# Kernel optimization log

Measured on AMD Instinct MI355X. Metric: run time of the kernel, lower is better.

The kernel has to match this reference:

```python
import jax, jax.numpy as jnp
import numpy as np

E = 1_000_000      # number of edges
T = 2_000_000      # number of angle triplets
EDGE_DIM = 64
HIDDEN = 128
LN_EPS = 1e-5


def _layer_norm(x, gamma, beta):
    mu = jnp.mean(x, axis=-1, keepdims=True)
    var = jnp.mean(jnp.square(x - mu), axis=-1, keepdims=True)
    return (x - mu) * jax.lax.rsqrt(var + LN_EPS) * gamma + beta


def setup_inputs() -> dict:
    key = jax.random.key(0)
    ks = jax.random.split(key, 8)
    in_dim = 2 * EDGE_DIM + 4  # 132

    def lin(k, fan_in, fan_out):
        bound = 1.0 / np.sqrt(fan_in)
        kw, kb = jax.random.split(k)
        W = jax.random.uniform(kw, (fan_in, fan_out), jnp.float32, -bound, bound)
        b = jax.random.uniform(kb, (fan_out,), jnp.float32, -bound, bound)
        return W, b

    W1, b1 = lin(ks[0], in_dim, HIDDEN)
    W2, b2 = lin(ks[1], HIDDEN, HIDDEN)
    W3, b3 = lin(ks[2], HIDDEN, EDGE_DIM)

    return {
        "edge_feat": jax.random.normal(ks[3], (E, EDGE_DIM), jnp.float32),
        "triplet_idx": jax.random.randint(ks[4], (T, 2), 0, E, jnp.int64) if jax.config.jax_enable_x64 else jax.random.randint(ks[4], (T, 2), 0, E, jnp.int32),
        "triplet_geo": jax.random.uniform(ks[5], (T, 4), jnp.float32),
        "W1": W1, "b1": b1,
        "g1": jnp.ones((HIDDEN,), jnp.float32), "be1": jnp.zeros((HIDDEN,), jnp.float32),
        "W2": W2, "b2": b2,
        "g2": jnp.ones((HIDDEN,), jnp.float32), "be2": jnp.zeros((HIDDEN,), jnp.float32),
        "W3": W3, "b3": b3,
        "gn": jnp.ones((EDGE_DIM,), jnp.float32), "bn": jnp.zeros((EDGE_DIM,), jnp.float32),
    }


def reference(edge_feat, triplet_idx, triplet_geo,
              W1, b1, g1, be1, W2, b2, g2, be2, W3, b3, gn, bn):
    num_edges = edge_feat.shape[0]
    e_ij = triplet_idx[:, 0]
    e_kj = triplet_idx[:, 1]

    f_ij = edge_feat[e_ij]                      # [T, edge_dim] gather
    f_kj = edge_feat[e_kj]                      # [T, edge_dim] gather
    x = jnp.concatenate([f_ij, f_kj, triplet_geo], axis=1)  # [T, 2*edge_dim+4]

    # mlp_phi: Linear -> SiLU -> LayerNorm -> Linear -> SiLU -> LayerNorm
    h = _layer_norm(jax.nn.silu(x @ W1 + b1), g1, be1)
    m = _layer_norm(jax.nn.silu(h @ W2 + b2), g2, be2)  # [T, hidden]

    # scatter-mean over e_ij with dim_size = num_edges
    sums = jax.ops.segment_sum(m, e_ij, num_segments=num_edges)
    cnts = jax.ops.segment_sum(jnp.ones((m.shape[0],), m.dtype), e_ij, num_segments=num_edges)
    agg = sums / jnp.maximum(cnts, 1.0)[:, None]         # [E, hidden]

    out = edge_feat + (agg @ W3 + b3)
    return _layer_norm(out, gn, bn)
```

## Files before the change

### kernel.cpp

```cpp
#include <hip/hip_runtime.h>
#include <hip/hip_bf16.h>
#include <stdint.h>

typedef __attribute__((ext_vector_type(8))) short short8;
typedef __attribute__((ext_vector_type(4))) float f32x4;
typedef unsigned short u16;

#define OFF_PSUM 0ULL
#define OFF_CNT  256000000ULL
#define OFF_EBF  260000000ULL
#define OFF_WT1  388000000ULL
#define OFF_WT2  (OFF_WT1 + 40960ULL)
#define OFF_WP3  (OFF_WT2 + 32768ULL)
#define OFF_S2   (OFF_WP3 + 16384ULL)
#define OFF_C2   (OFF_S2 + 512ULL)
#define OFF_S3   (OFF_C2 + 512ULL)
#define OFF_T3   (OFF_S3 + 256ULL)

#define LDS_HM   0
#define LDS_TAIL 16384
#define LDS_P1S  20480
#define LDS_P1Q  20992
#define LDS_P2S  21504
#define LDS_P2Q  22016
#define LDS_EIJ  22528
#define LDS_TOTAL 22784

__device__ __forceinline__ u16 f2bf(float f) {
  union { float f; uint32_t u; } c; c.f = f;
  uint32_t u = c.u;
  return (u16)((u + 0x7FFFu + ((u >> 16) & 1u)) >> 16);
}
__device__ __forceinline__ uint32_t pkbf(float lo, float hi) {
  float2 t; t.x = lo; t.y = hi;
  __hip_bfloat162 h = __float22bfloat162_rn(t);
  uint32_t u; __builtin_memcpy(&u, &h, 4);
  return u;
}
__device__ __forceinline__ float silu(float y) {
  return y * __builtin_amdgcn_rcpf(1.0f + __expf(-y));
}

#define MFMA16(a, b, c) __builtin_amdgcn_mfma_f32_16x16x32_bf16((a), (b), (c), 0, 0, 0)


__global__ __launch_bounds__(256) void k_conv_edge(const float* __restrict__ ef,
                                                   u16* __restrict__ ebf) {
  int i = blockIdx.x * 256 + threadIdx.x;
  float4 v = ((const float4*)ef)[i];
  ushort4 o;
  o.x = f2bf(v.x); o.y = f2bf(v.y); o.z = f2bf(v.z); o.w = f2bf(v.w);
  ((ushort4*)ebf)[i] = o;
}

__global__ __launch_bounds__(256) void k_pack_w(const float* __restrict__ W1,
                                                const float* __restrict__ W2,
                                                const float* __restrict__ W3,
                                                const float* __restrict__ g1,
                                                const float* __restrict__ g2,
                                                u16* __restrict__ wt1,
                                                u16* __restrict__ wt2,
                                                u16* __restrict__ wp3) {
  int i = blockIdx.x * 256 + threadIdx.x;
  if (i < 20480) {
    int n = i / 160, k = i - n * 160;
    wt1[i] = (k < 132) ? f2bf(W1[k * 128 + n]) : (u16)0;
  } else if (i < 36864) {
    int i2 = i - 20480;
    int n = i2 >> 7, k = i2 & 127;
    wt2[i2] = f2bf(g1[k] * W2[k * 128 + n]);
  } else if (i < 45056) {
    int i3 = i - 36864;
    int j = i3 & 7, n = (i3 >> 3) & 63, kb = i3 >> 9;
    int k = kb * 8 + j;
    wp3[i3] = f2bf(g2[k] * W3[k * 64 + n]);
  }
}

__global__ __launch_bounds__(256) void k_pack_vec(
    const float* __restrict__ W2, const float* __restrict__ W3,
    const float* __restrict__ g1, const float* __restrict__ be1, const float* __restrict__ b2,
    const float* __restrict__ g2, const float* __restrict__ be2,
    float* __restrict__ s2, float* __restrict__ c2,
    float* __restrict__ s3, float* __restrict__ t3) {
  int t = threadIdx.x;
  if (t < 128) {
    float a = 0.f, b = 0.f;
    for (int k = 0; k < 128; ++k) {
      float w = W2[k * 128 + t];
      a += g1[k] * w; b += be1[k] * w;
    }
    s2[t] = a; c2[t] = b + b2[t];
  } else if (t < 192) {
    int n = t - 128;
    float a = 0.f, b = 0.f;
    for (int k = 0; k < 128; ++k) {
      float w = W3[k * 64 + n];
      a += g2[k] * w; b += be2[k] * w;
    }
    s3[n] = a; t3[n] = b;
  }
}


__global__ __launch_bounds__(256, 5) void k_triplet(
    const u16* __restrict__ ebf, const int* __restrict__ tidx,
    const float* __restrict__ geo,
    const u16* __restrict__ wt1, const u16* __restrict__ wt2, const u16* __restrict__ wp3,
    const float* __restrict__ b1,
    const float* __restrict__ s2v, const float* __restrict__ c2v,
    const float* __restrict__ s3v,
    float* __restrict__ psum, float* __restrict__ cnt) {
  __shared__ __align__(16) char smem[LDS_TOTAL];
  float* P1S = (float*)(smem + LDS_P1S);
  float* P1Q = (float*)(smem + LDS_P1Q);
  float* P2S = (float*)(smem + LDS_P2S);
  float* P2Q = (float*)(smem + LDS_P2Q);
  int* EIJ = (int*)(smem + LDS_EIJ);

  const int tid = threadIdx.x;
  const int wave = tid >> 6, lane = tid & 63;
  const int wm = wave >> 1, wn = wave & 1;
  const int l15 = lane & 15, lg = lane >> 4;
  const int t0 = blockIdx.x * 64;

  const int tA = wn * 32 + l15;
  const int tB = tA + 16;
  int2 pA = ((const int2*)tidx)[t0 + tA];
  int2 pB = ((const int2*)tidx)[t0 + tB];

  const short8* eb = (const short8*)ebf;
  short8 bxA0 = eb[(size_t)pA.x * 8 + lg];
  short8 bxA1 = eb[(size_t)pA.x * 8 + 4 + lg];
  short8 bxA2 = eb[(size_t)pA.y * 8 + lg];
  short8 bxA3 = eb[(size_t)pA.y * 8 + 4 + lg];
  short8 bxB0 = eb[(size_t)pB.x * 8 + lg];
  short8 bxB1 = eb[(size_t)pB.x * 8 + 4 + lg];
  short8 bxB2 = eb[(size_t)pB.y * 8 + lg];
  short8 bxB3 = eb[(size_t)pB.y * 8 + 4 + lg];

  if (tid < 64) {
    int2 p = ((const int2*)tidx)[t0 + tid];
    EIJ[tid] = p.x;
    atomicAdd(&cnt[p.x], 1.0f);
    float4 gq = ((const float4*)geo)[t0 + tid];
    uint2 gw; gw.x = pkbf(gq.x, gq.y); gw.y = pkbf(gq.z, gq.w);
    char* tp = smem + LDS_TAIL + tid * 64;
    const int ts = (tid & 3) << 4;
    *(uint2*)(tp + (0 ^ ts)) = gw;
    *(uint2*)(tp + (0 ^ ts) + 8) = (uint2){0, 0};
    *(uint4*)(tp + (16 ^ ts)) = (uint4){0, 0, 0, 0};
    *(uint4*)(tp + (32 ^ ts)) = (uint4){0, 0, 0, 0};
    *(uint4*)(tp + (48 ^ ts)) = (uint4){0, 0, 0, 0};
  }
  __syncthreads();

  short8 btA = *(const short8*)(smem + LDS_TAIL + tA * 64 + ((lg * 16) ^ ((tA & 3) << 4)));
  short8 btB = *(const short8*)(smem + LDS_TAIL + tB * 64 + ((lg * 16) ^ ((tB & 3) << 4)));

  f32x4 acc[4][2];
#pragma unroll
  for (int mf = 0; mf < 4; ++mf) { acc[mf][0] = (f32x4)0.f; acc[mf][1] = (f32x4)0.f; }
  const short8* w1p = (const short8*)wt1;
#pragma unroll
  for (int s5 = 0; s5 < 5; ++s5) {
    short8 b0, b1x;
    if (s5 == 0) { b0 = bxA0; b1x = bxB0; }
    else if (s5 == 1) { b0 = bxA1; b1x = bxB1; }
    else if (s5 == 2) { b0 = bxA2; b1x = bxB2; }
    else if (s5 == 3) { b0 = bxA3; b1x = bxB3; }
    else { b0 = btA; b1x = btB; }
#pragma unroll
    for (int mf = 0; mf < 4; ++mf) {
      short8 aw = w1p[(wm * 64 + mf * 16 + l15) * 20 + s5 * 4 + lg];
      acc[mf][0] = MFMA16(aw, b0, acc[mf][0]);
      acc[mf][1] = MFMA16(aw, b1x, acc[mf][1]);
    }
  }

  {
    float4 b1f[4];
#pragma unroll
    for (int mf = 0; mf < 4; ++mf)
      b1f[mf] = *(const float4*)(b1 + wm * 64 + mf * 16 + lg * 4);
    float st[2] = {0.f, 0.f}, sq[2] = {0.f, 0.f};
#pragma unroll
    for (int mf = 0; mf < 4; ++mf)
#pragma unroll
      for (int f = 0; f < 2; ++f)
#pragma unroll
        for (int q = 0; q < 4; ++q) {
          float v = silu(acc[mf][f][q] + b1f[mf][q]);
          acc[mf][f][q] = v;
          st[f] += v; sq[f] += v * v;
        }
#pragma unroll
    for (int f = 0; f < 2; ++f) {
      st[f] += __shfl_xor(st[f], 16); sq[f] += __shfl_xor(sq[f], 16);
      st[f] += __shfl_xor(st[f], 32); sq[f] += __shfl_xor(sq[f], 32);
    }
    if (lg == 0) {
#pragma unroll
      for (int f = 0; f < 2; ++f) {
        int trip = wn * 32 + f * 16 + l15;
        P1S[trip * 2 + wm] = st[f];
        P1Q[trip * 2 + wm] = sq[f];
      }
    }
#pragma unroll
    for (int mf = 0; mf < 4; ++mf)
#pragma unroll
      for (int f = 0; f < 2; ++f) {
        int trip = wn * 32 + f * 16 + l15;
        uint2 w;
        w.x = pkbf(acc[mf][f][0], acc[mf][f][1]);
        w.y = pkbf(acc[mf][f][2], acc[mf][f][3]);
        *(uint2*)(smem + LDS_HM + trip * 256 +
                  ((wm * 128 + mf * 32 + lg * 8) ^ ((trip & 7) << 4))) = w;
      }
  }
  __syncthreads();

#pragma unroll
  for (int mf = 0; mf < 4; ++mf) { acc[mf][0] = (f32x4)0.f; acc[mf][1] = (f32x4)0.f; }
  const short8* w2p = (const short8*)wt2;
#pragma unroll
  for (int s4 = 0; s4 < 4; ++s4) {
    short8 bx0, bx1;
    {
      int trip = wn * 32 + l15;
      bx0 = *(const short8*)(smem + LDS_HM + trip * 256 +
                             ((s4 * 64 + lg * 16) ^ ((trip & 7) << 4)));
      int trip2 = trip + 16;
      bx1 = *(const short8*)(smem + LDS_HM + trip2 * 256 +
                             ((s4 * 64 + lg * 16) ^ ((trip2 & 7) << 4)));
    }
#pragma unroll
    for (int mf = 0; mf < 4; ++mf) {
      short8 aw = w2p[(wm * 64 + mf * 16 + l15) * 16 + s4 * 4 + lg];
      acc[mf][0] = MFMA16(aw, bx0, acc[mf][0]);
      acc[mf][1] = MFMA16(aw, bx1, acc[mf][1]);
    }
  }

  {
    float4 s2f[4], c2f[4];
#pragma unroll
    for (int mf = 0; mf < 4; ++mf) {
      s2f[mf] = *(const float4*)(s2v + wm * 64 + mf * 16 + lg * 4);
      c2f[mf] = *(const float4*)(c2v + wm * 64 + mf * 16 + lg * 4);
    }
    float mu[2], inv[2];
#pragma unroll
    for (int f = 0; f < 2; ++f) {
      int trip = wn * 32 + f * 16 + l15;
      float sm = P1S[trip * 2] + P1S[trip * 2 + 1];
      float qq = P1Q[trip * 2] + P1Q[trip * 2 + 1];
      mu[f] = sm * 0.0078125f;
      inv[f] = rsqrtf(fmaxf(qq * 0.0078125f - mu[f] * mu[f], 0.f) + 1e-5f);
    }
    float st[2] = {0.f, 0.f}, sq[2] = {0.f, 0.f};
#pragma unroll
    for (int mf = 0; mf < 4; ++mf)
#pragma unroll
      for (int f = 0; f < 2; ++f)
#pragma unroll
        for (int q = 0; q < 4; ++q) {
          float y = inv[f] * (acc[mf][f][q] - mu[f] * s2f[mf][q]) + c2f[mf][q];
          float v = silu(y);
          acc[mf][f][q] = v;
          st[f] += v; sq[f] += v * v;
        }
#pragma unroll
    for (int f = 0; f < 2; ++f) {
      st[f] += __shfl_xor(st[f], 16); sq[f] += __shfl_xor(sq[f], 16);
      st[f] += __shfl_xor(st[f], 32); sq[f] += __shfl_xor(sq[f], 32);
    }
    if (lg == 0) {
#pragma unroll
      for (int f = 0; f < 2; ++f) {
        int trip = wn * 32 + f * 16 + l15;
        P2S[trip * 2 + wm] = st[f];
        P2Q[trip * 2 + wm] = sq[f];
      }
    }
  }
  __syncthreads();

#pragma unroll
  for (int mf = 0; mf < 4; ++mf)
#pragma unroll
    for (int f = 0; f < 2; ++f) {
      int trip = wn * 32 + f * 16 + l15;
      uint2 w;
      w.x = pkbf(acc[mf][f][0], acc[mf][f][1]);
      w.y = pkbf(acc[mf][f][2], acc[mf][f][3]);
      *(uint2*)(smem + LDS_HM + trip * 256 +
                ((wm * 128 + mf * 32 + lg * 8) ^ ((trip & 7) << 4))) = w;
    }
  __syncthreads();

  f32x4 acc3[4];
#pragma unroll
  for (int nf = 0; nf < 4; ++nf) acc3[nf] = (f32x4)0.f;
  const short8* wb3 = (const short8*)wp3;
#pragma unroll
  for (int s4 = 0; s4 < 4; ++s4) {
    int row = wave * 16 + l15;
    short8 a = *(const short8*)(smem + LDS_HM + row * 256 +
                                ((s4 * 64 + lg * 16) ^ ((row & 7) << 4)));
#pragma unroll
    for (int nf = 0; nf < 4; ++nf) {
      short8 b = wb3[(s4 * 4 + lg) * 64 + nf * 16 + l15];
      acc3[nf] = MFMA16(a, b, acc3[nf]);
    }
  }
  {
    float s3c[4];
#pragma unroll
    for (int nf = 0; nf < 4; ++nf) s3c[nf] = s3v[nf * 16 + l15];
#pragma unroll
    for (int q = 0; q < 4; ++q) {
      int row = wave * 16 + lg * 4 + q;
      float sm = P2S[row * 2] + P2S[row * 2 + 1];
      float qq = P2Q[row * 2] + P2Q[row * 2 + 1];
      float mu = sm * 0.0078125f;
      float inv = rsqrtf(fmaxf(qq * 0.0078125f - mu * mu, 0.f) + 1e-5f);
      float* base = psum + (size_t)EIJ[row] * 64;
#pragma unroll
      for (int nf = 0; nf < 4; ++nf) {
        float y = inv * (acc3[nf][q] - mu * s3c[nf]);
        atomicAdd(base + nf * 16 + l15, y);
      }
    }
  }
}


__global__ __launch_bounds__(256) void k_final(
    const float* __restrict__ psum, const float* __restrict__ cnt,
    const float* __restrict__ ef, const float* __restrict__ b3,
    const float* __restrict__ t3, const float* __restrict__ gn,
    const float* __restrict__ bn, float* __restrict__ out) {
  int g = blockIdx.x * 256 + threadIdx.x;
  int e = g >> 2, s = g & 3;
  float cv = cnt[e];
  float ic = 1.0f / fmaxf(cv, 1.0f);
  float tw = (cv > 0.f) ? 1.0f : 0.0f;
  float x[16];
  const float4* ps = (const float4*)(psum + (size_t)e * 64 + s * 16);
  const float4* fe = (const float4*)(ef + (size_t)e * 64 + s * 16);
  const float4* p3 = (const float4*)(b3 + s * 16);
  const float4* pt = (const float4*)(t3 + s * 16);
#pragma unroll
  for (int i = 0; i < 4; ++i) {
    float4 a = ps[i], b = fe[i], c = p3[i], d = pt[i];
    x[4 * i + 0] = b.x + a.x * ic + c.x + tw * d.x;
    x[4 * i + 1] = b.y + a.y * ic + c.y + tw * d.y;
    x[4 * i + 2] = b.z + a.z * ic + c.z + tw * d.z;
    x[4 * i + 3] = b.w + a.w * ic + c.w + tw * d.w;
  }
  float sum = 0.f, ss = 0.f;
#pragma unroll
  for (int i = 0; i < 16; ++i) { sum += x[i]; ss += x[i] * x[i]; }
  sum += __shfl_xor(sum, 1); ss += __shfl_xor(ss, 1);
  sum += __shfl_xor(sum, 2); ss += __shfl_xor(ss, 2);
  float mu = sum * (1.0f / 64.0f);
  float inv = rsqrtf(ss * (1.0f / 64.0f) - mu * mu + 1e-5f);
  float4* po = (float4*)(out + (size_t)e * 64 + s * 16);
#pragma unroll
  for (int i = 0; i < 4; ++i) {
    float4 gv = ((const float4*)(gn + s * 16))[i];
    float4 bv = ((const float4*)(bn + s * 16))[i];
    float4 o;
    o.x = (x[4 * i + 0] - mu) * inv * gv.x + bv.x;
    o.y = (x[4 * i + 1] - mu) * inv * gv.y + bv.y;
    o.z = (x[4 * i + 2] - mu) * inv * gv.z + bv.z;
    o.w = (x[4 * i + 3] - mu) * inv * gv.w + bv.w;
    po[i] = o;
  }
}

extern "C" void kernel_launch(void* const* d_in, const int* in_sizes, int n_in,
                              void* d_out, int out_size, void* d_ws, size_t ws_size,
                              hipStream_t stream) {
  const float* edge_feat = (const float*)d_in[0];
  const int* tidx = (const int*)d_in[1];
  const float* geo = (const float*)d_in[2];
  const float* W1 = (const float*)d_in[3];
  const float* b1 = (const float*)d_in[4];
  const float* g1 = (const float*)d_in[5];
  const float* be1 = (const float*)d_in[6];
  const float* W2 = (const float*)d_in[7];
  const float* b2 = (const float*)d_in[8];
  const float* g2 = (const float*)d_in[9];
  const float* be2 = (const float*)d_in[10];
  const float* W3 = (const float*)d_in[11];
  const float* b3 = (const float*)d_in[12];
  const float* gn = (const float*)d_in[13];
  const float* bn = (const float*)d_in[14];

  char* ws = (char*)d_ws;
  float* psum = (float*)(ws + OFF_PSUM);
  float* cnt = (float*)(ws + OFF_CNT);
  u16* ebf = (u16*)(ws + OFF_EBF);
  u16* wt1 = (u16*)(ws + OFF_WT1);
  u16* wt2 = (u16*)(ws + OFF_WT2);
  u16* wp3 = (u16*)(ws + OFF_WP3);
  float* s2 = (float*)(ws + OFF_S2);
  float* c2 = (float*)(ws + OFF_C2);
  float* s3 = (float*)(ws + OFF_S3);
  float* t3 = (float*)(ws + OFF_T3);
  float* out = (float*)d_out;

  hipMemsetAsync(ws, 0, 260000000ULL, stream);
  k_conv_edge<<<62500, 256, 0, stream>>>(edge_feat, ebf);
  k_pack_w<<<176, 256, 0, stream>>>(W1, W2, W3, g1, g2, wt1, wt2, wp3);
  k_pack_vec<<<1, 256, 0, stream>>>(W2, W3, g1, be1, b2, g2, be2, s2, c2, s3, t3);

  k_triplet<<<31250, 256, 0, stream>>>(ebf, tidx, geo, wt1, wt2, wp3,
                                       b1, s2, c2, s3, psum, cnt);
  k_final<<<15625, 256, 0, stream>>>(psum, cnt, edge_feat, b3, t3, gn, bn, out);
}
```

Measured before the change: 1.063 ms.

## Replace atomic scatter-mean with counting sort and segmented reduction

```diff
diff --git a/kernel.cpp b/kernel.cpp
--- a/kernel.cpp
+++ b/kernel.cpp
@@ -6,16 +6,24 @@
 typedef __attribute__((ext_vector_type(4))) float f32x4;
 typedef unsigned short u16;
 
-#define OFF_PSUM 0ULL
-#define OFF_CNT  256000000ULL
-#define OFF_EBF  260000000ULL
+#define N_E 1000000
+#define N_T 2000000
+#define NB_SCAN 3907
+
+#define OFF_MBUF 0ULL
+#define OFF_EBF  256000000ULL
+#define OFF_CUR  384000000ULL
 #define OFF_WT1  388000000ULL
 #define OFF_WT2  (OFF_WT1 + 40960ULL)
-#define OFF_WP3  (OFF_WT2 + 32768ULL)
-#define OFF_S2   (OFF_WP3 + 16384ULL)
+#define OFF_WT3  (OFF_WT2 + 32768ULL)
+#define OFF_S2   (OFF_WT3 + 16384ULL)
 #define OFF_C2   (OFF_S2 + 512ULL)
 #define OFF_S3   (OFF_C2 + 512ULL)
 #define OFF_T3   (OFF_S3 + 256ULL)
+
+#define DO_HIST    0ULL
+#define DO_SORTEDT 4000000ULL
+#define DO_BSUM    12000000ULL
 
 #define LDS_HM   0
 #define LDS_TAIL 16384
@@ -23,8 +31,7 @@
 #define LDS_P1Q  20992
 #define LDS_P2S  21504
 #define LDS_P2Q  22016
-#define LDS_EIJ  22528
-#define LDS_TOTAL 22784
+#define LDS_TOTAL 22528
 
 __device__ __forceinline__ u16 f2bf(float f) {
   union { float f; uint32_t u; } c; c.f = f;
@@ -36,6 +43,12 @@
   __hip_bfloat162 h = __float22bfloat162_rn(t);
   uint32_t u; __builtin_memcpy(&u, &h, 4);
   return u;
+}
+__device__ __forceinline__ float blo(uint32_t u) {
+  union { uint32_t u; float f; } c; c.u = u << 16; return c.f;
+}
+__device__ __forceinline__ float bhi(uint32_t u) {
+  union { uint32_t u; float f; } c; c.u = u & 0xffff0000u; return c.f;
 }
 __device__ __forceinline__ float silu(float y) {
   return y * __builtin_amdgcn_rcpf(1.0f + __expf(-y));
@@ -60,7 +73,7 @@
                                                 const float* __restrict__ g2,
                                                 u16* __restrict__ wt1,
                                                 u16* __restrict__ wt2,
-                                                u16* __restrict__ wp3) {
+                                                u16* __restrict__ wt3) {
   int i = blockIdx.x * 256 + threadIdx.x;
   if (i < 20480) {
     int n = i / 160, k = i - n * 160;
@@ -71,9 +84,8 @@
     wt2[i2] = f2bf(g1[k] * W2[k * 128 + n]);
   } else if (i < 45056) {
     int i3 = i - 36864;
-    int j = i3 & 7, n = (i3 >> 3) & 63, kb = i3 >> 9;
-    int k = kb * 8 + j;
-    wp3[i3] = f2bf(g2[k] * W3[k * 64 + n]);
+    int n = i3 >> 7, k = i3 & 127;
+    wt3[i3] = f2bf(g2[k] * W3[k * 64 + n]);
   }
 }
 
@@ -103,31 +115,104 @@
 }
 
 
-__global__ __launch_bounds__(256, 5) void k_triplet(
-    const u16* __restrict__ ebf, const int* __restrict__ tidx,
-    const float* __restrict__ geo,
-    const u16* __restrict__ wt1, const u16* __restrict__ wt2, const u16* __restrict__ wp3,
+__global__ __launch_bounds__(256) void k_hist(const int2* __restrict__ tidx,
+                                              int* __restrict__ hist) {
+  int t = blockIdx.x * 256 + threadIdx.x;
+  if (t < N_T) atomicAdd(&hist[tidx[t].x], 1);
+}
+
+__global__ __launch_bounds__(256) void k_scan_bsum(const int* __restrict__ hist,
+                                                   int* __restrict__ bsum) {
+  int b = blockIdx.x, tid = threadIdx.x;
+  int i = b * 256 + tid;
+  int v = (i < N_E) ? hist[i] : 0;
+#pragma unroll
+  for (int d = 1; d < 64; d <<= 1) v += __shfl_xor(v, d);
+  __shared__ int ws4[4];
+  if ((tid & 63) == 0) ws4[tid >> 6] = v;
+  __syncthreads();
+  if (tid == 0) bsum[b] = ws4[0] + ws4[1] + ws4[2] + ws4[3];
+}
+
+__global__ __launch_bounds__(256) void k_scan_boffs(int* __restrict__ bsum, int nb) {
+  __shared__ int ws4[4];
+  __shared__ int carry;
+  int tid = threadIdx.x, lane = tid & 63, w = tid >> 6;
+  if (tid == 0) carry = 0;
+  __syncthreads();
+  for (int base = 0; base < nb; base += 256) {
+    int i = base + tid;
+    int v = (i < nb) ? bsum[i] : 0;
+    int inc = v;
+#pragma unroll
+    for (int d = 1; d < 64; d <<= 1) { int u = __shfl_up(inc, d); if (lane >= d) inc += u; }
+    if (lane == 63) ws4[w] = inc;
+    __syncthreads();
+    int off = 0;
+    for (int k = 0; k < w; ++k) off += ws4[k];
+    int excl = carry + off + inc - v;
+    int total = ws4[0] + ws4[1] + ws4[2] + ws4[3];
+    __syncthreads();
+    if (i < nb) bsum[i] = excl;
+    if (tid == 0) carry += total;
+    __syncthreads();
+  }
+}
+
+__global__ __launch_bounds__(256) void k_scan_fin(const int* __restrict__ hist,
+                                                  const int* __restrict__ bsum,
+                                                  int* __restrict__ cursor) {
+  int b = blockIdx.x, tid = threadIdx.x, lane = tid & 63, w = tid >> 6;
+  int i = b * 256 + tid;
+  int v = (i < N_E) ? hist[i] : 0;
+  int inc = v;
+#pragma unroll
+  for (int d = 1; d < 64; d <<= 1) { int u = __shfl_up(inc, d); if (lane >= d) inc += u; }
+  __shared__ int ws4[4];
+  if (lane == 63) ws4[w] = inc;
+  __syncthreads();
+  int off = 0;
+  for (int k = 0; k < w; ++k) off += ws4[k];
+  if (i < N_E) cursor[i] = bsum[b] + off + inc - v;
+}
+
+__global__ __launch_bounds__(256) void k_scatter(const int2* __restrict__ tidx,
+                                                 int* __restrict__ cursor,
+                                                 int* __restrict__ sortedT) {
+  int t = blockIdx.x * 256 + threadIdx.x;
+  if (t < N_T) {
+    int pos = atomicAdd(&cursor[tidx[t].x], 1);
+    sortedT[pos] = t;
+  }
+}
+
+
+__global__ __launch_bounds__(256, 4) void k_triplet(
+    const u16* __restrict__ ebf, const int2* __restrict__ tidx,
+    const float4* __restrict__ geo4, const int* __restrict__ sortedT,
+    const u16* __restrict__ wt1, const u16* __restrict__ wt2, const u16* __restrict__ wt3,
     const float* __restrict__ b1,
     const float* __restrict__ s2v, const float* __restrict__ c2v,
     const float* __restrict__ s3v,
-    float* __restrict__ psum, float* __restrict__ cnt) {
+    u16* __restrict__ mbuf) {
   __shared__ __align__(16) char smem[LDS_TOTAL];
   float* P1S = (float*)(smem + LDS_P1S);
   float* P1Q = (float*)(smem + LDS_P1Q);
   float* P2S = (float*)(smem + LDS_P2S);
   float* P2Q = (float*)(smem + LDS_P2Q);
-  int* EIJ = (int*)(smem + LDS_EIJ);
 
   const int tid = threadIdx.x;
   const int wave = tid >> 6, lane = tid & 63;
   const int wm = wave >> 1, wn = wave & 1;
   const int l15 = lane & 15, lg = lane >> 4;
-  const int t0 = blockIdx.x * 64;
+  const int i0 = blockIdx.x * 64;
 
   const int tA = wn * 32 + l15;
   const int tB = tA + 16;
-  int2 pA = ((const int2*)tidx)[t0 + tA];
-  int2 pB = ((const int2*)tidx)[t0 + tB];
+  int stA = sortedT[i0 + tA];
+  int stB = sortedT[i0 + tB];
+  int2 pA = tidx[stA];
+  int2 pB = tidx[stB];
 
   const short8* eb = (const short8*)ebf;
   short8 bxA0 = eb[(size_t)pA.x * 8 + lg];
@@ -140,10 +225,8 @@
   short8 bxB3 = eb[(size_t)pB.y * 8 + 4 + lg];
 
   if (tid < 64) {
-    int2 p = ((const int2*)tidx)[t0 + tid];
-    EIJ[tid] = p.x;
-    atomicAdd(&cnt[p.x], 1.0f);
-    float4 gq = ((const float4*)geo)[t0 + tid];
+    int st = sortedT[i0 + tid];
+    float4 gq = geo4[st];
     uint2 gw; gw.x = pkbf(gq.x, gq.y); gw.y = pkbf(gq.z, gq.w);
     char* tp = smem + LDS_TAIL + tid * 64;
     const int ts = (tid & 3) << 4;
@@ -300,37 +383,52 @@
     }
   __syncthreads();
 
-  f32x4 acc3[4];
-#pragma unroll
-  for (int nf = 0; nf < 4; ++nf) acc3[nf] = (f32x4)0.f;
-  const short8* wb3 = (const short8*)wp3;
+  f32x4 acc3[2][2];
+#pragma unroll
+  for (int mf = 0; mf < 2; ++mf) { acc3[mf][0] = (f32x4)0.f; acc3[mf][1] = (f32x4)0.f; }
+  const short8* w3p = (const short8*)wt3;
 #pragma unroll
   for (int s4 = 0; s4 < 4; ++s4) {
-    int row = wave * 16 + l15;
-    short8 a = *(const short8*)(smem + LDS_HM + row * 256 +
-                                ((s4 * 64 + lg * 16) ^ ((row & 7) << 4)));
-#pragma unroll
-    for (int nf = 0; nf < 4; ++nf) {
-      short8 b = wb3[(s4 * 4 + lg) * 64 + nf * 16 + l15];
-      acc3[nf] = MFMA16(a, b, acc3[nf]);
-    }
-  }
+    short8 bx0, bx1;
+    {
+      int trip = wn * 32 + l15;
+      bx0 = *(const short8*)(smem + LDS_HM + trip * 256 +
+                             ((s4 * 64 + lg * 16) ^ ((trip & 7) << 4)));
+      int trip2 = trip + 16;
+      bx1 = *(const short8*)(smem + LDS_HM + trip2 * 256 +
+                             ((s4 * 64 + lg * 16) ^ ((trip2 & 7) << 4)));
+    }
+#pragma unroll
+    for (int mf = 0; mf < 2; ++mf) {
+      short8 aw = w3p[(wm * 32 + mf * 16 + l15) * 16 + s4 * 4 + lg];
+      acc3[mf][0] = MFMA16(aw, bx0, acc3[mf][0]);
+      acc3[mf][1] = MFMA16(aw, bx1, acc3[mf][1]);
+    }
+  }
+
   {
-    float s3c[4];
-#pragma unroll
-    for (int nf = 0; nf < 4; ++nf) s3c[nf] = s3v[nf * 16 + l15];
-#pragma unroll
-    for (int q = 0; q < 4; ++q) {
-      int row = wave * 16 + lg * 4 + q;
-      float sm = P2S[row * 2] + P2S[row * 2 + 1];
-      float qq = P2Q[row * 2] + P2Q[row * 2 + 1];
-      float mu = sm * 0.0078125f;
-      float inv = rsqrtf(fmaxf(qq * 0.0078125f - mu * mu, 0.f) + 1e-5f);
-      float* base = psum + (size_t)EIJ[row] * 64;
-#pragma unroll
-      for (int nf = 0; nf < 4; ++nf) {
-        float y = inv * (acc3[nf][q] - mu * s3c[nf]);
-        atomicAdd(base + nf * 16 + l15, y);
+    float4 s3f[2];
+#pragma unroll
+    for (int mf = 0; mf < 2; ++mf)
+      s3f[mf] = *(const float4*)(s3v + wm * 32 + mf * 16 + lg * 4);
+#pragma unroll
+    for (int f = 0; f < 2; ++f) {
+      int trip = wn * 32 + f * 16 + l15;
+      float sm = P2S[trip * 2] + P2S[trip * 2 + 1];
+      float qq = P2Q[trip * 2] + P2Q[trip * 2 + 1];
+      float mu3 = sm * 0.0078125f;
+      float inv3 = rsqrtf(fmaxf(qq * 0.0078125f - mu3 * mu3, 0.f) + 1e-5f);
+      u16* rowp = mbuf + (size_t)(i0 + trip) * 64;
+#pragma unroll
+      for (int mf = 0; mf < 2; ++mf) {
+        float y0 = inv3 * (acc3[mf][f][0] - mu3 * s3f[mf][0]);
+        float y1 = inv3 * (acc3[mf][f][1] - mu3 * s3f[mf][1]);
+        float y2 = inv3 * (acc3[mf][f][2] - mu3 * s3f[mf][2]);
+        float y3 = inv3 * (acc3[mf][f][3] - mu3 * s3f[mf][3]);
+        uint2 w;
+        w.x = pkbf(y0, y1);
+        w.y = pkbf(y2, y3);
+        *(uint2*)(rowp + wm * 32 + mf * 16 + lg * 4) = w;
       }
     }
   }
@@ -338,27 +436,39 @@
 
 
 __global__ __launch_bounds__(256) void k_final(
-    const float* __restrict__ psum, const float* __restrict__ cnt,
+    const u16* __restrict__ mbuf, const int* __restrict__ cursor,
     const float* __restrict__ ef, const float* __restrict__ b3,
     const float* __restrict__ t3, const float* __restrict__ gn,
     const float* __restrict__ bn, float* __restrict__ out) {
   int g = blockIdx.x * 256 + threadIdx.x;
   int e = g >> 2, s = g & 3;
-  float cv = cnt[e];
-  float ic = 1.0f / fmaxf(cv, 1.0f);
-  float tw = (cv > 0.f) ? 1.0f : 0.0f;
+  int end = cursor[e];
+  int start = (e > 0) ? cursor[e - 1] : 0;
+  int c = end - start;
+  float ic = 1.0f / (float)((c > 0) ? c : 1);
+  float tw = (c > 0) ? 1.0f : 0.0f;
+  float a[16];
+#pragma unroll
+  for (int i = 0; i < 16; ++i) a[i] = 0.f;
+  for (int r = start; r < end; ++r) {
+    const uint4* mp = (const uint4*)(mbuf + (size_t)r * 64 + s * 16);
+    uint4 u0 = mp[0], u1 = mp[1];
+    a[0] += blo(u0.x); a[1] += bhi(u0.x); a[2] += blo(u0.y); a[3] += bhi(u0.y);
+    a[4] += blo(u0.z); a[5] += bhi(u0.z); a[6] += blo(u0.w); a[7] += bhi(u0.w);
+    a[8] += blo(u1.x); a[9] += bhi(u1.x); a[10] += blo(u1.y); a[11] += bhi(u1.y);
+    a[12] += blo(u1.z); a[13] += bhi(u1.z); a[14] += blo(u1.w); a[15] += bhi(u1.w);
+  }
   float x[16];
-  const float4* ps = (const float4*)(psum + (size_t)e * 64 + s * 16);
   const float4* fe = (const float4*)(ef + (size_t)e * 64 + s * 16);
   const float4* p3 = (const float4*)(b3 + s * 16);
   const float4* pt = (const float4*)(t3 + s * 16);
 #pragma unroll
   for (int i = 0; i < 4; ++i) {
-    float4 a = ps[i], b = fe[i], c = p3[i], d = pt[i];
-    x[4 * i + 0] = b.x + a.x * ic + c.x + tw * d.x;
-    x[4 * i + 1] = b.y + a.y * ic + c.y + tw * d.y;
-    x[4 * i + 2] = b.z + a.z * ic + c.z + tw * d.z;
-    x[4 * i + 3] = b.w + a.w * ic + c.w + tw * d.w;
+    float4 b = fe[i], cc = p3[i], d = pt[i];
+    x[4 * i + 0] = b.x + a[4 * i + 0] * ic + cc.x + tw * d.x;
+    x[4 * i + 1] = b.y + a[4 * i + 1] * ic + cc.y + tw * d.y;
+    x[4 * i + 2] = b.z + a[4 * i + 2] * ic + cc.z + tw * d.z;
+    x[4 * i + 3] = b.w + a[4 * i + 3] * ic + cc.w + tw * d.w;
   }
   float sum = 0.f, ss = 0.f;
 #pragma unroll
@@ -385,8 +495,8 @@
                               void* d_out, int out_size, void* d_ws, size_t ws_size,
                               hipStream_t stream) {
   const float* edge_feat = (const float*)d_in[0];
-  const int* tidx = (const int*)d_in[1];
-  const float* geo = (const float*)d_in[2];
+  const int2* tidx = (const int2*)d_in[1];
+  const float4* geo4 = (const float4*)d_in[2];
   const float* W1 = (const float*)d_in[3];
   const float* b1 = (const float*)d_in[4];
   const float* g1 = (const float*)d_in[5];
@@ -401,24 +511,35 @@
   const float* bn = (const float*)d_in[14];
 
   char* ws = (char*)d_ws;
-  float* psum = (float*)(ws + OFF_PSUM);
-  float* cnt = (float*)(ws + OFF_CNT);
+  u16* mbuf = (u16*)(ws + OFF_MBUF);
   u16* ebf = (u16*)(ws + OFF_EBF);
+  int* cursor = (int*)(ws + OFF_CUR);
   u16* wt1 = (u16*)(ws + OFF_WT1);
   u16* wt2 = (u16*)(ws + OFF_WT2);
-  u16* wp3 = (u16*)(ws + OFF_WP3);
+  u16* wt3 = (u16*)(ws + OFF_WT3);
   float* s2 = (float*)(ws + OFF_S2);
   float* c2 = (float*)(ws + OFF_C2);
   float* s3 = (float*)(ws + OFF_S3);
   float* t3 = (float*)(ws + OFF_T3);
+
+  char* ob = (char*)d_out;
+  int* hist = (int*)(ob + DO_HIST);
+  int* sortedT = (int*)(ob + DO_SORTEDT);
+  int* bsum = (int*)(ob + DO_BSUM);
   float* out = (float*)d_out;
 
-  hipMemsetAsync(ws, 0, 260000000ULL, stream);
+  hipMemsetAsync(hist, 0, (size_t)N_E * 4, stream);
   k_conv_edge<<<62500, 256, 0, stream>>>(edge_feat, ebf);
-  k_pack_w<<<176, 256, 0, stream>>>(W1, W2, W3, g1, g2, wt1, wt2, wp3);
+  k_pack_w<<<176, 256, 0, stream>>>(W1, W2, W3, g1, g2, wt1, wt2, wt3);
   k_pack_vec<<<1, 256, 0, stream>>>(W2, W3, g1, be1, b2, g2, be2, s2, c2, s3, t3);
 
-  k_triplet<<<31250, 256, 0, stream>>>(ebf, tidx, geo, wt1, wt2, wp3,
-                                       b1, s2, c2, s3, psum, cnt);
-  k_final<<<15625, 256, 0, stream>>>(psum, cnt, edge_feat, b3, t3, gn, bn, out);
-}
+  k_hist<<<7813, 256, 0, stream>>>(tidx, hist);
+  k_scan_bsum<<<NB_SCAN, 256, 0, stream>>>(hist, bsum);
+  k_scan_boffs<<<1, 256, 0, stream>>>(bsum, NB_SCAN);
+  k_scan_fin<<<NB_SCAN, 256, 0, stream>>>(hist, bsum, cursor);
+  k_scatter<<<7813, 256, 0, stream>>>(tidx, cursor, sortedT);
+
+  k_triplet<<<31250, 256, 0, stream>>>(ebf, tidx, geo4, sortedT,
+                                       wt1, wt2, wt3, b1, s2, c2, s3, mbuf);
+  k_final<<<15625, 256, 0, stream>>>(mbuf, cursor, edge_feat, b3, t3, gn, bn, out);
+}
```

Result: slower. 1.209 ms (+13.7%).
